# Kernel tuning notes

Hardware: AMD Instinct MI355X
Metric: run time of the kernel (lower is better)

## Reference

```python
import jax, jax.numpy as jnp
import numpy as np

B, T, C, H = 4, 4096, 1024, 16


def setup_inputs() -> dict:
    key = jax.random.key(0)
    k1, k2, k3 = jax.random.split(key, 3)
    x = jax.random.normal(k1, (B, T, C), dtype=jnp.float32)
    # nn.Linear(d_model, 3*d_model, bias=False): weight shape [3C, C]
    W_qkv = jax.random.normal(k2, (3 * C, C), dtype=jnp.float32) * 0.02
    # output Linear(d_model, d_model): weight [C, C], bias [C]
    W_out = jax.random.normal(k3, (C, C), dtype=jnp.float32) * 0.02
    b_out = jnp.zeros((C,), dtype=jnp.float32)
    return {"x": x, "W_qkv": W_qkv, "W_out": W_out, "b_out": b_out}


def reference(x, W_qkv, W_out, b_out):
    Bs, Ts, Cs = x.shape
    dh = Cs // H
    scale = dh ** (-0.5)
    # qkv projection: [B,T,3C]
    qkv = x @ W_qkv.T
    q, k, v = jnp.split(qkv, 3, axis=-1)

    def to_heads(t):  # [B,T,C] -> [B,H,T,dh]
        return t.reshape(Bs, Ts, H, dh).transpose(0, 2, 1, 3)

    q, k, v = to_heads(q), to_heads(k), to_heads(v)
    # rfft over the sequence dim -> [B,H,F,dh], F = T//2+1 (complex64)
    q_f = jnp.fft.rfft(q, axis=-2)
    k_f = jnp.fft.rfft(k, axis=-2)
    # spectral score: sum over head_dim of conj(q)*k, real part -> [B,H,F]
    attn = jnp.sum(jnp.conj(q_f) * k_f, axis=-1).real * scale
    attn = jax.nn.softmax(attn, axis=-1)  # softmax over frequency bins
    v_f = jnp.fft.rfft(v, axis=-2)
    out = jnp.fft.irfft(attn[..., None] * v_f, n=Ts, axis=-2)  # [B,H,T,dh]
    out = out.transpose(0, 2, 1, 3).reshape(Bs, Ts, Cs)
    # output projection (dropout is identity in eval)
    return out @ W_out.T + b_out
```

## Files before the change

### kernel.cpp

```cpp
#include <hip/hip_runtime.h>
#include <math.h>

#define Bsz   4
#define Tsz   4096
#define Csz   1024
#define Hn    16
#define DHn   64
#define NTOT  (Bsz * Tsz)
#define M3    (3 * Csz)
#define Fn    2049
#define BHn   (Bsz * Hn)
#define HALFN 8192

typedef __bf16 bf16x8 __attribute__((ext_vector_type(8)));
typedef __bf16 bf16x4 __attribute__((ext_vector_type(4)));
typedef float  f32x4  __attribute__((ext_vector_type(4)));

#define VMCNT(n) asm volatile("s_waitcnt vmcnt(" #n ")" ::: "memory")
#define LGKM0    asm volatile("s_waitcnt lgkmcnt(0)" ::: "memory")

__device__ __forceinline__ void gload_lds16(const void* g, void* l) {
  __builtin_amdgcn_global_load_lds(
      (const __attribute__((address_space(1))) void*)g,
      (__attribute__((address_space(3))) void*)l, 16, 0, 0);
}

__global__ __launch_bounds__(256)
void cvt_hilo_kernel(const float4* __restrict__ in, bf16x4* __restrict__ hi,
                     bf16x4* __restrict__ lo, int n4) {
  int i = blockIdx.x * blockDim.x + threadIdx.x;
  if (i >= n4) return;
  float4 v = in[i];
  bf16x4 h, l;
  h[0] = (__bf16)v.x; h[1] = (__bf16)v.y; h[2] = (__bf16)v.z; h[3] = (__bf16)v.w;
  l[0] = (__bf16)(v.x - (float)h[0]);
  l[1] = (__bf16)(v.y - (float)h[1]);
  l[2] = (__bf16)(v.z - (float)h[2]);
  l[3] = (__bf16)(v.w - (float)h[3]);
  hi[i] = h;
  lo[i] = l;
}

__global__ __launch_bounds__(256)
void transpose_cvt_kernel(const float* __restrict__ src,
                          __bf16* __restrict__ hi, __bf16* __restrict__ lo) {
  __shared__ float tile[64][65];
  const int tid = threadIdx.x;
  const int n0 = blockIdx.x * 64;
  const int c0 = blockIdx.y * 64;
  const int col = tid & 63;
  const int row4 = tid >> 6;
#pragma unroll
  for (int i = 0; i < 16; ++i) {
    const int r = i * 4 + row4;
    tile[r][col] = src[(size_t)(c0 + r) * NTOT + n0 + col];
  }
  __syncthreads();
#pragma unroll
  for (int i = 0; i < 16; ++i) {
    const int n = i * 4 + row4;
    const float v = tile[col][n];
    const __bf16 h = (__bf16)v;
    const __bf16 l = (__bf16)(v - (float)h);
    hi[(size_t)(n0 + n) * Csz + c0 + col] = h;
    lo[(size_t)(n0 + n) * Csz + c0 + col] = l;
  }
}

template<int COLMAP>
__global__ __launch_bounds__(512, 2)
void gemm_8s(const __bf16* __restrict__ Ahi, const __bf16* __restrict__ Alo,
             const __bf16* __restrict__ Bhi, const __bf16* __restrict__ Blo,
             float* __restrict__ C, int ldC, int nbase,
             const float* __restrict__ bias) {
  __shared__ __align__(16) char lds[131072];

  const int tid  = threadIdx.x;
  const int wid  = tid >> 6;
  const int lane = tid & 63;
  const int wm = wid >> 2, wn = wid & 3;

  int bx = blockIdx.x, by = blockIdx.y;
  {
    const int gx = gridDim.x, gy = gridDim.y;
    const int nwg = gx * gy;
    if ((nwg & 7) == 0) {
      const int flat  = by * gx + bx;
      const int chunk = nwg >> 3;
      const int nf    = (flat & 7) * chunk + (flat >> 3);
      if (COLMAP) { bx = nf / gy; by = nf % gy; }
      else        { bx = nf % gx; by = nf / gx; }
    }
  }
  const int m0 = by * 256;
  const int n0 = bx * 256;

  const int r16 = lane & 15;
  const int kc  = lane >> 4;

  const int aq = (wid & 3) + ((wid & 4) ? 4 : 0);
  const int bq = ((wid & 3) << 1) + (wid >> 2);
  const __bf16* gAh = Ahi + (size_t)(m0 + (wid & 3) * 16 + ((wid & 4) ? 128 : 0) + r16) * Csz + kc * 8;
  const __bf16* gAl = Alo + (size_t)(m0 + (wid & 3) * 16 + ((wid & 4) ? 128 : 0) + r16) * Csz + kc * 8;
  const __bf16* gBh = Bhi + (size_t)(n0 + (wid & 3) * 64 + (wid >> 2) * 16 + r16) * Csz + kc * 8;
  const __bf16* gBl = Blo + (size_t)(n0 + (wid & 3) * 64 + (wid >> 2) * 16 + r16) * Csz + kc * 8;

  auto stA = [&](int h, int ts, char* slot) {
    const size_t o = (size_t)h * 64 * Csz + ts * 32;
    gload_lds16(gAh + o, slot + aq * 1024);
    gload_lds16(gAl + o, slot + 8192 + aq * 1024);
  };
  auto stB = [&](int h, int ts, char* slot) {
    const size_t o = (size_t)h * 32 * Csz + ts * 32;
    gload_lds16(gBh + o, slot + bq * 1024);
    gload_lds16(gBl + o, slot + 8192 + bq * 1024);
  };

  f32x4 acc[8][4];
#pragma unroll
  for (int i = 0; i < 8; ++i)
#pragma unroll
    for (int j = 0; j < 4; ++j) acc[i][j] = (f32x4)(0.f);

  stA(0, 0, lds);            stB(0, 0, lds + 16384);
  stB(1, 0, lds + 32768);    stA(1, 0, lds + 49152);
  stA(0, 1, lds + 65536);    stB(0, 1, lds + 81920);

#pragma unroll 1
  for (int t = 0; t < 32; ++t) {
    char* cur = lds + ((t & 1) << 16);
    char* nxt = lds + (((t & 1) ^ 1) << 16);
    bf16x8 ah[4], al[4], bh[4], bl[4];

    if (t < 31) { VMCNT(8); } else { VMCNT(4); }
    __builtin_amdgcn_s_barrier();
#pragma unroll
    for (int f = 0; f < 4; ++f) {
      const int off = (wm * 4 + f) * 1024 + lane * 16;
      ah[f] = *(const bf16x8*)(cur + off);
      al[f] = *(const bf16x8*)(cur + 8192 + off);
    }
#pragma unroll
    for (int j = 0; j < 2; ++j) {
      const int off = ((wn << 1) + j) * 1024 + lane * 16;
      bh[j] = *(const bf16x8*)(cur + 16384 + off);
      bl[j] = *(const bf16x8*)(cur + 16384 + 8192 + off);
    }
    if (t < 31) stB(1, t + 1, nxt + 32768);
    LGKM0;
    __builtin_amdgcn_sched_barrier(0);
    __builtin_amdgcn_s_setprio(1);
#pragma unroll
    for (int f = 0; f < 4; ++f)
#pragma unroll
      for (int j = 0; j < 2; ++j) {
        f32x4 a_ = acc[f][j];
        a_ = __builtin_amdgcn_mfma_f32_16x16x32_bf16(ah[f], bh[j], a_, 0, 0, 0);
        a_ = __builtin_amdgcn_mfma_f32_16x16x32_bf16(ah[f], bl[j], a_, 0, 0, 0);
        a_ = __builtin_amdgcn_mfma_f32_16x16x32_bf16(al[f], bh[j], a_, 0, 0, 0);
        acc[f][j] = a_;
      }
    __builtin_amdgcn_s_setprio(0);

    if (t < 31) { VMCNT(8); } else { VMCNT(2); }
    __builtin_amdgcn_s_barrier();
#pragma unroll
    for (int j = 0; j < 2; ++j) {
      const int off = ((wn << 1) + j) * 1024 + lane * 16;
      bh[2 + j] = *(const bf16x8*)(cur + 32768 + off);
      bl[2 + j] = *(const bf16x8*)(cur + 32768 + 8192 + off);
    }
    if (t < 31) stA(1, t + 1, nxt + 49152);
    LGKM0;
    __builtin_amdgcn_sched_barrier(0);
    __builtin_amdgcn_s_setprio(1);
#pragma unroll
    for (int f = 0; f < 4; ++f)
#pragma unroll
      for (int j = 0; j < 2; ++j) {
        f32x4 a_ = acc[f][2 + j];
        a_ = __builtin_amdgcn_mfma_f32_16x16x32_bf16(ah[f], bh[2 + j], a_, 0, 0, 0);
        a_ = __builtin_amdgcn_mfma_f32_16x16x32_bf16(ah[f], bl[2 + j], a_, 0, 0, 0);
        a_ = __builtin_amdgcn_mfma_f32_16x16x32_bf16(al[f], bh[2 + j], a_, 0, 0, 0);
        acc[f][2 + j] = a_;
      }
    __builtin_amdgcn_s_setprio(0);

    if (t < 31) { VMCNT(8); } else { VMCNT(0); }
    __builtin_amdgcn_s_barrier();
#pragma unroll
    for (int f = 0; f < 4; ++f) {
      const int off = (wm * 4 + f) * 1024 + lane * 16;
      ah[f] = *(const bf16x8*)(cur + 49152 + off);
      al[f] = *(const bf16x8*)(cur + 49152 + 8192 + off);
    }
    if (t < 30) stA(0, t + 2, cur);
    LGKM0;
    __builtin_amdgcn_sched_barrier(0);
    __builtin_amdgcn_s_setprio(1);
#pragma unroll
    for (int f = 0; f < 4; ++f)
#pragma unroll
      for (int j = 0; j < 2; ++j) {
        f32x4 a_ = acc[4 + f][j];
        a_ = __builtin_amdgcn_mfma_f32_16x16x32_bf16(ah[f], bh[j], a_, 0, 0, 0);
        a_ = __builtin_amdgcn_mfma_f32_16x16x32_bf16(ah[f], bl[j], a_, 0, 0, 0);
        a_ = __builtin_amdgcn_mfma_f32_16x16x32_bf16(al[f], bh[j], a_, 0, 0, 0);
        acc[4 + f][j] = a_;
      }
    __builtin_amdgcn_s_setprio(0);

    __builtin_amdgcn_s_barrier();
    if (t < 30) stB(0, t + 2, cur + 16384);
    __builtin_amdgcn_s_setprio(1);
#pragma unroll
    for (int f = 0; f < 4; ++f)
#pragma unroll
      for (int j = 0; j < 2; ++j) {
        f32x4 a_ = acc[4 + f][2 + j];
        a_ = __builtin_amdgcn_mfma_f32_16x16x32_bf16(ah[f], bh[2 + j], a_, 0, 0, 0);
        a_ = __builtin_amdgcn_mfma_f32_16x16x32_bf16(ah[f], bl[2 + j], a_, 0, 0, 0);
        a_ = __builtin_amdgcn_mfma_f32_16x16x32_bf16(al[f], bh[2 + j], a_, 0, 0, 0);
        acc[4 + f][2 + j] = a_;
      }
    __builtin_amdgcn_s_setprio(0);
  }

  const int cm = m0 + wm * 128 + (lane >> 4) * 4;
  const int cn = nbase + n0 + wn * 64 + (lane & 15);
  float bb[4];
#pragma unroll
  for (int g = 0; g < 4; ++g) bb[g] = bias ? bias[cn - nbase + g * 16] : 0.f;
#pragma unroll
  for (int fm = 0; fm < 8; ++fm)
#pragma unroll
    for (int r = 0; r < 4; ++r) {
      float* cp = C + (size_t)(cm + fm * 16 + r) * ldC + cn;
#pragma unroll
      for (int g = 0; g < 4; ++g) cp[g * 16] = acc[fm][g][r] + bb[g];
    }
}

template<int COLMAP>
__global__ __launch_bounds__(512, 2)
void gemm_8s4(const __bf16* __restrict__ Ahi, const __bf16* __restrict__ Alo,
              const __bf16* __restrict__ Bhi, const __bf16* __restrict__ Blo,
              float* __restrict__ C, int ldC, int nbase,
              const float* __restrict__ bias) {
  __shared__ __align__(16) char lds[98304];

  const int tid  = threadIdx.x;
  const int wid  = tid >> 6;
  const int lane = tid & 63;
  const int wm = wid >> 2, wn = wid & 3;

  int bx = blockIdx.x, by = blockIdx.y;
  {
    const int gx = gridDim.x, gy = gridDim.y;
    const int nwg = gx * gy;
    if ((nwg & 7) == 0) {
      const int flat  = by * gx + bx;
      const int chunk = nwg >> 3;
      const int nf    = (flat & 7) * chunk + (flat >> 3);
      if (COLMAP) { bx = nf / gy; by = nf % gy; }
      else        { bx = nf % gx; by = nf / gx; }
    }
  }
  const int m0 = by * 128;
  const int n0 = bx * 256;

  const int r16 = lane & 15;
  const int kc  = lane >> 4;

  const int cw = wid & 3;
  const __bf16* gA = ((wid & 4) ? Alo : Ahi) +
      (size_t)(m0 + (cw >> 1) * 64 + (cw & 1) * 16 + r16) * Csz + kc * 8;
  const int adst = ((wid & 4) ? 4096 : 0) + cw * 1024;
  const int bq = ((wid & 3) << 1) + (wid >> 2);
  const __bf16* gBh = Bhi + (size_t)(n0 + (wid & 3) * 64 + (wid >> 2) * 16 + r16) * Csz + kc * 8;
  const __bf16* gBl = Blo + (size_t)(n0 + (wid & 3) * 64 + (wid >> 2) * 16 + r16) * Csz + kc * 8;

  auto stA = [&](int h, int ts, char* slot) {
    gload_lds16(gA + (size_t)h * 32 * Csz + ts * 32, slot + adst);
  };
  auto stB = [&](int h, int ts, char* slot) {
    const size_t o = (size_t)h * 32 * Csz + ts * 32;
    gload_lds16(gBh + o, slot + bq * 1024);
    gload_lds16(gBl + o, slot + 8192 + bq * 1024);
  };

  f32x4 acc[4][4];
#pragma unroll
  for (int i = 0; i < 4; ++i)
#pragma unroll
    for (int j = 0; j < 4; ++j) acc[i][j] = (f32x4)(0.f);

  stA(0, 0, lds);            stB(0, 0, lds + 8192);
  stB(1, 0, lds + 24576);    stA(1, 0, lds + 40960);
  stA(0, 1, lds + 49152);    stB(0, 1, lds + 49152 + 8192);

#pragma unroll 1
  for (int t = 0; t < 32; ++t) {
    char* cur = lds + (t & 1) * 49152;
    char* nxt = lds + ((t & 1) ^ 1) * 49152;
    bf16x8 ah[2], al[2], bh[4], bl[4];

    if (t < 31) { VMCNT(6); } else { VMCNT(3); }
    __builtin_amdgcn_s_barrier();
#pragma unroll
    for (int f = 0; f < 2; ++f) {
      const int off = (wm * 2 + f) * 1024 + lane * 16;
      ah[f] = *(const bf16x8*)(cur + off);
      al[f] = *(const bf16x8*)(cur + 4096 + off);
    }
#pragma unroll
    for (int j = 0; j < 2; ++j) {
      const int off = ((wn << 1) + j) * 1024 + lane * 16;
      bh[j] = *(const bf16x8*)(cur + 8192 + off);
      bl[j] = *(const bf16x8*)(cur + 8192 + 8192 + off);
    }
    if (t < 31) stB(1, t + 1, nxt + 24576);
    LGKM0;
    __builtin_amdgcn_sched_barrier(0);
    __builtin_amdgcn_s_setprio(1);
#pragma unroll
    for (int f = 0; f < 2; ++f)
#pragma unroll
      for (int j = 0; j < 2; ++j) {
        f32x4 a_ = acc[f][j];
        a_ = __builtin_amdgcn_mfma_f32_16x16x32_bf16(ah[f], bh[j], a_, 0, 0, 0);
        a_ = __builtin_amdgcn_mfma_f32_16x16x32_bf16(ah[f], bl[j], a_, 0, 0, 0);
        a_ = __builtin_amdgcn_mfma_f32_16x16x32_bf16(al[f], bh[j], a_, 0, 0, 0);
        acc[f][j] = a_;
      }
    __builtin_amdgcn_s_setprio(0);

    if (t < 31) { VMCNT(6); } else { VMCNT(1); }
    __builtin_amdgcn_s_barrier();
#pragma unroll
    for (int j = 0; j < 2; ++j) {
      const int off = ((wn << 1) + j) * 1024 + lane * 16;
      bh[2 + j] = *(const bf16x8*)(cur + 24576 + off);
      bl[2 + j] = *(const bf16x8*)(cur + 24576 + 8192 + off);
    }
    if (t < 31) stA(1, t + 1, nxt + 40960);
    LGKM0;
    __builtin_amdgcn_sched_barrier(0);
    __builtin_amdgcn_s_setprio(1);
#pragma unroll
    for (int f = 0; f < 2; ++f)
#pragma unroll
      for (int j = 0; j < 2; ++j) {
        f32x4 a_ = acc[f][2 + j];
        a_ = __builtin_amdgcn_mfma_f32_16x16x32_bf16(ah[f], bh[2 + j], a_, 0, 0, 0);
        a_ = __builtin_amdgcn_mfma_f32_16x16x32_bf16(ah[f], bl[2 + j], a_, 0, 0, 0);
        a_ = __builtin_amdgcn_mfma_f32_16x16x32_bf16(al[f], bh[2 + j], a_, 0, 0, 0);
        acc[f][2 + j] = a_;
      }
    __builtin_amdgcn_s_setprio(0);

    if (t < 31) { VMCNT(6); } else { VMCNT(0); }
    __builtin_amdgcn_s_barrier();
#pragma unroll
    for (int f = 0; f < 2; ++f) {
      const int off = (wm * 2 + f) * 1024 + lane * 16;
      ah[f] = *(const bf16x8*)(cur + 40960 + off);
      al[f] = *(const bf16x8*)(cur + 40960 + 4096 + off);
    }
    if (t < 30) stA(0, t + 2, cur);
    LGKM0;
    __builtin_amdgcn_sched_barrier(0);
    __builtin_amdgcn_s_setprio(1);
#pragma unroll
    for (int f = 0; f < 2; ++f)
#pragma unroll
      for (int j = 0; j < 2; ++j) {
        f32x4 a_ = acc[2 + f][j];
        a_ = __builtin_amdgcn_mfma_f32_16x16x32_bf16(ah[f], bh[j], a_, 0, 0, 0);
        a_ = __builtin_amdgcn_mfma_f32_16x16x32_bf16(ah[f], bl[j], a_, 0, 0, 0);
        a_ = __builtin_amdgcn_mfma_f32_16x16x32_bf16(al[f], bh[j], a_, 0, 0, 0);
        acc[2 + f][j] = a_;
      }
    __builtin_amdgcn_s_setprio(0);

    __builtin_amdgcn_s_barrier();
    if (t < 30) stB(0, t + 2, cur + 8192);
    __builtin_amdgcn_s_setprio(1);
#pragma unroll
    for (int f = 0; f < 2; ++f)
#pragma unroll
      for (int j = 0; j < 2; ++j) {
        f32x4 a_ = acc[2 + f][2 + j];
        a_ = __builtin_amdgcn_mfma_f32_16x16x32_bf16(ah[f], bh[2 + j], a_, 0, 0, 0);
        a_ = __builtin_amdgcn_mfma_f32_16x16x32_bf16(ah[f], bl[2 + j], a_, 0, 0, 0);
        a_ = __builtin_amdgcn_mfma_f32_16x16x32_bf16(al[f], bh[2 + j], a_, 0, 0, 0);
        acc[2 + f][2 + j] = a_;
      }
    __builtin_amdgcn_s_setprio(0);
  }

  const int cm = m0 + wm * 64 + (lane >> 4) * 4;
  const int cn = nbase + n0 + wn * 64 + (lane & 15);
  float bb[4];
#pragma unroll
  for (int g = 0; g < 4; ++g) bb[g] = bias ? bias[cn - nbase + g * 16] : 0.f;
#pragma unroll
  for (int fm = 0; fm < 4; ++fm)
#pragma unroll
    for (int r = 0; r < 4; ++r) {
      float* cp = C + (size_t)(cm + fm * 16 + r) * ldC + cn;
#pragma unroll
      for (int g = 0; g < 4; ++g) cp[g * 16] = acc[fm][g][r] + bb[g];
    }
}

template<int NT>
__device__ __forceinline__ void build_twiddle(float2* tw, int tid) {
  const float k = 6.28318530717958647692f / 4096.0f;
#pragma unroll
  for (int i = 0; i < 1024 / NT; ++i) {
    const int e = tid + i * NT;
    float sn, cs;
    __sincosf(k * (float)e, &sn, &cs);
    tw[e] = make_float2(cs, sn);
  }
}

__device__ __forceinline__ float2 cmul(float2 a, float2 b) {
  return make_float2(a.x * b.x - a.y * b.y, a.x * b.y + a.y * b.x);
}

template<int NT>
__device__ __forceinline__ void fft4096_r4(float2* X, float2* Y,
                                           const float2* __restrict__ tw,
                                           int tid, float sign) {
  float2* src = X;
  float2* dst = Y;
#pragma unroll 1
  for (int stage = 0; stage < 6; ++stage) {
    const int s = 1 << (2 * stage);
    __syncthreads();
#pragma unroll
    for (int it = 0; it < 1024 / NT; ++it) {
      const int idx = tid + it * NT;
      const int sp = idx & ~(s - 1);
      float2 a0 = src[idx];
      float2 a1 = src[idx + 1024];
      float2 a2 = src[idx + 2048];
      float2 a3 = src[idx + 3072];
      float2 b0 = make_float2(a0.x + a2.x, a0.y + a2.y);
      float2 b1 = make_float2(a0.x - a2.x, a0.y - a2.y);
      float2 b2 = make_float2(a1.x + a3.x, a1.y + a3.y);
      float2 b3 = make_float2(a1.x - a3.x, a1.y - a3.y);
      float2 y0 = make_float2(b0.x + b2.x, b0.y + b2.y);
      float2 y2 = make_float2(b0.x - b2.x, b0.y - b2.y);
      float2 y1 = make_float2(b1.x - sign * b3.y, b1.y + sign * b3.x);
      float2 y3 = make_float2(b1.x + sign * b3.y, b1.y - sign * b3.x);
      float2 w1 = tw[sp];
      w1.y *= sign;
      float2 w2 = make_float2(w1.x * w1.x - w1.y * w1.y, 2.f * w1.x * w1.y);
      float2 w3 = cmul(w1, w2);
      const int o = idx + 3 * sp;
      dst[o]         = y0;
      dst[o + s]     = cmul(w1, y1);
      dst[o + 2 * s] = cmul(w2, y2);
      dst[o + 3 * s] = cmul(w3, y3);
    }
    float2* t = src; src = dst; dst = t;
  }
  __syncthreads();
}

__global__ __launch_bounds__(512)
void qk_cross_kernel(const float* __restrict__ qkT, float* __restrict__ attn_raw,
                     int bhbase) {
  __shared__ float2 bufA[4096];
  __shared__ float2 bufB[4096];
  __shared__ float2 twid[1024];
  const int tid = threadIdx.x;
  const int blk = blockIdx.x;
  const int d = blk & 63;
  const int bh = bhbase + (blk >> 6);
  const int h = bh & 15;
  const int b = bh >> 4;

  build_twiddle<512>(twid, tid);

  const float4* qrow = (const float4*)(qkT + (size_t)(h * DHn + d) * NTOT + b * Tsz);
  const float4* krow = (const float4*)(qkT + (size_t)(Csz + h * DHn + d) * NTOT + b * Tsz);
#pragma unroll
  for (int i = 0; i < 2; ++i) {
    const int t4 = tid + (i << 9);
    float4 qv = qrow[t4];
    float4 kv = krow[t4];
    bufA[t4 * 4 + 0] = make_float2(qv.x, kv.x);
    bufA[t4 * 4 + 1] = make_float2(qv.y, kv.y);
    bufA[t4 * 4 + 2] = make_float2(qv.z, kv.z);
    bufA[t4 * 4 + 3] = make_float2(qv.w, kv.w);
  }

  fft4096_r4<512>(bufA, bufB, twid, tid, -1.0f);

  float* outp = attn_raw + (size_t)bh * Fn;
  for (int f = tid; f < Fn; f += 512) {
    float2 zf = bufA[f];
    float2 zn = bufA[(4096 - f) & 4095];
    float ar = zf.x + zn.x;
    float ai = zf.y - zn.y;
    float br = zf.x - zn.x;
    float bi = zf.y + zn.y;
    float val = 0.03125f * (ar * bi - ai * br);
    atomicAdd(&outp[f], val);
  }
}

__global__ __launch_bounds__(256)
void softmax_kernel(const float* __restrict__ raw, float* __restrict__ attn) {
  __shared__ float red[256];
  const int tid = threadIdx.x;
  const float* in = raw + (size_t)blockIdx.x * Fn;
  float* outp = attn + (size_t)blockIdx.x * Fn;

  float lmax = -3.4e38f;
  for (int f = tid; f < Fn; f += 256) lmax = fmaxf(lmax, in[f]);
  red[tid] = lmax;
  __syncthreads();
  for (int off = 128; off > 0; off >>= 1) {
    if (tid < off) red[tid] = fmaxf(red[tid], red[tid + off]);
    __syncthreads();
  }
  const float mx = red[0];
  __syncthreads();

  float lsum = 0.f;
  for (int f = tid; f < Fn; f += 256) lsum += __expf(in[f] - mx);
  red[tid] = lsum;
  __syncthreads();
  for (int off = 128; off > 0; off >>= 1) {
    if (tid < off) red[tid] += red[tid + off];
    __syncthreads();
  }
  const float inv = 1.0f / red[0];
  for (int f = tid; f < Fn; f += 256) outp[f] = __expf(in[f] - mx) * inv;
}

__global__ __launch_bounds__(512)
void v_filter_kernel(const float* __restrict__ vT, float* __restrict__ vbarT,
                     const float* __restrict__ attn) {
  __shared__ float2 bufA[4096];
  __shared__ float2 bufB[4096];
  __shared__ float2 twid[1024];
  const int tid = threadIdx.x;
  const int blk = blockIdx.x;
  const int jp = blk & 31;
  const int bh = blk >> 5;
  const int h = bh & 15;
  const int b = bh >> 4;
  const int d0 = jp * 2;

  build_twiddle<512>(twid, tid);

  const float4* v0 = (const float4*)(vT + (size_t)(h * DHn + d0) * NTOT + b * Tsz);
  const float4* v1 = (const float4*)(vT + (size_t)(h * DHn + d0 + 1) * NTOT + b * Tsz);
#pragma unroll
  for (int i = 0; i < 2; ++i) {
    const int t4 = tid + (i << 9);
    float4 av = v0[t4];
    float4 bv = v1[t4];
    bufA[t4 * 4 + 0] = make_float2(av.x, bv.x);
    bufA[t4 * 4 + 1] = make_float2(av.y, bv.y);
    bufA[t4 * 4 + 2] = make_float2(av.z, bv.z);
    bufA[t4 * 4 + 3] = make_float2(av.w, bv.w);
  }

  fft4096_r4<512>(bufA, bufB, twid, tid, -1.0f);

  const float* a = attn + (size_t)bh * Fn;
  for (int f = tid; f < 4096; f += 512) {
    int fm = (f <= 2048) ? f : (4096 - f);
    float s = a[fm];
    float2 z = bufA[f];
    bufA[f] = make_float2(z.x * s, z.y * s);
  }

  fft4096_r4<512>(bufA, bufB, twid, tid, +1.0f);

  float* y0 = vbarT + (size_t)(h * DHn + d0) * NTOT + b * Tsz;
  float* y1 = y0 + NTOT;
  const float inv = 1.0f / 4096.0f;
  for (int t = tid; t < 4096; t += 512) {
    float2 z = bufA[t];
    y0[t] = z.x * inv;
    y1[t] = z.y * inv;
  }
}

__global__ void zero_kernel(float* __restrict__ p, int n) {
  int i = blockIdx.x * blockDim.x + threadIdx.x;
  if (i < n) p[i] = 0.f;
}

extern "C" void kernel_launch(void* const* d_in, const int* in_sizes, int n_in,
                              void* d_out, int out_size, void* d_ws, size_t ws_size,
                              hipStream_t stream) {
  const float* x    = (const float*)d_in[0];
  const float* Wqkv = (const float*)d_in[1];
  const float* Wout = (const float*)d_in[2];
  const float* bout = (const float*)d_in[3];
  float* out = (float*)d_out;

  char* ws = (char*)d_ws;
  float* qkT      = (float*)ws;
  float* vT       = (float*)ws;
  __bf16* VThi    = (__bf16*)ws;
  __bf16* VTlo    = (__bf16*)(ws + 33554432ull);
  float* vbarT    = (float*)(ws + 67108864ull);
  float* attn_raw = (float*)(ws + 134217728ull);
  float* attn     = (float*)(ws + 134742272ull);
  __bf16* Whi     = (__bf16*)(ws + 135266816ull);
  __bf16* Wlo     = (__bf16*)(ws + 141558272ull);
  __bf16* Xhi     = (__bf16*)(ws + 147849728ull);
  __bf16* Xlo     = (__bf16*)(ws + 164626944ull);
  __bf16* Wouthi  = (__bf16*)(ws + 181404160ull);
  __bf16* Woutlo  = (__bf16*)(ws + 183501312ull);

  const int nraw = BHn * Fn;
  zero_kernel<<<(nraw + 255) / 256, 256, 0, stream>>>(attn_raw, nraw);

  cvt_hilo_kernel<<<3072, 256, 0, stream>>>((const float4*)Wqkv,
                                            (bf16x4*)Whi, (bf16x4*)Wlo, 786432);
  cvt_hilo_kernel<<<1024, 256, 0, stream>>>((const float4*)Wout,
                                            (bf16x4*)Wouthi, (bf16x4*)Woutlo, 262144);

  for (int half = 0; half < 2; ++half) {
    cvt_hilo_kernel<<<8192, 256, 0, stream>>>(
        (const float4*)(x + (size_t)half * HALFN * Csz),
        (bf16x4*)Xhi, (bf16x4*)Xlo, 2097152);
    gemm_8s<1><<<dim3(32, 8), 512, 0, stream>>>(Whi, Wlo, Xhi, Xlo,
                                                qkT, NTOT, half * HALFN, nullptr);
    qk_cross_kernel<<<2048, 512, 0, stream>>>(qkT, attn_raw, half * 32);
    gemm_8s4<1><<<dim3(32, 8), 512, 0, stream>>>(Whi + 2048 * Csz, Wlo + 2048 * Csz,
                                                 Xhi, Xlo, vT, NTOT, half * HALFN,
                                                 nullptr);
  }

  softmax_kernel<<<BHn, 256, 0, stream>>>(attn_raw, attn);

  v_filter_kernel<<<2048, 512, 0, stream>>>(vT, vbarT, attn);

  transpose_cvt_kernel<<<dim3(NTOT / 64, Csz / 64), 256, 0, stream>>>(vbarT, VThi, VTlo);

  gemm_8s<0><<<dim3(4, 64), 512, 0, stream>>>(VThi, VTlo, Wouthi, Woutlo,
                                              out, Csz, 0, bout);
}
```

Baseline: 553.7 us.

## Switch split-bf16 GEMM to 32x32x16 MFMA tiles with matching LDS layout

Rewrites the main three-pass bf16 hi/lo GEMM to use 32x32x16 MFMA instructions instead of 16x16x32. The global-to-LDS staging layout and the per-wave fragment loads change to feed 32-row tiles, and the epilogue is adapted to the 32x32 accumulator layout. The aim is fewer MFMA issues and fewer LDS fragment reads per FLOP, giving more operand reuse. The cost is a different store pattern in the epilogue and a risk of layout mismatches in the new index math.

```diff
diff --git a/kernel.cpp b/kernel.cpp
--- a/kernel.cpp
+++ b/kernel.cpp
@@ -15,6 +15,7 @@
 typedef __bf16 bf16x8 __attribute__((ext_vector_type(8)));
 typedef __bf16 bf16x4 __attribute__((ext_vector_type(4)));
 typedef float  f32x4  __attribute__((ext_vector_type(4)));
+typedef float  f32x16 __attribute__((ext_vector_type(16)));
 
 #define VMCNT(n) asm volatile("s_waitcnt vmcnt(" #n ")" ::: "memory")
 #define LGKM0    asm volatile("s_waitcnt lgkmcnt(0)" ::: "memory")
@@ -69,7 +70,7 @@
 
 template<int COLMAP>
 __global__ __launch_bounds__(512, 2)
-void gemm_8s(const __bf16* __restrict__ Ahi, const __bf16* __restrict__ Alo,
+void gemm_8w(const __bf16* __restrict__ Ahi, const __bf16* __restrict__ Alo,
              const __bf16* __restrict__ Bhi, const __bf16* __restrict__ Blo,
              float* __restrict__ C, int ldC, int nbase,
              const float* __restrict__ bias) {
@@ -95,20 +96,21 @@
   const int m0 = by * 256;
   const int n0 = bx * 256;
 
-  const int r16 = lane & 15;
-  const int kc  = lane >> 4;
-
-  const int aq = (wid & 3) + ((wid & 4) ? 4 : 0);
-  const int bq = ((wid & 3) << 1) + (wid >> 2);
-  const __bf16* gAh = Ahi + (size_t)(m0 + (wid & 3) * 16 + ((wid & 4) ? 128 : 0) + r16) * Csz + kc * 8;
-  const __bf16* gAl = Alo + (size_t)(m0 + (wid & 3) * 16 + ((wid & 4) ? 128 : 0) + r16) * Csz + kc * 8;
-  const __bf16* gBh = Bhi + (size_t)(n0 + (wid & 3) * 64 + (wid >> 2) * 16 + r16) * Csz + kc * 8;
-  const __bf16* gBl = Blo + (size_t)(n0 + (wid & 3) * 64 + (wid >> 2) * 16 + r16) * Csz + kc * 8;
+  const int r32 = lane & 31;
+  const int kc2 = lane >> 5;
+
+  const __bf16* gAh = Ahi + (size_t)(m0 + (wid >> 2) * 128 + ((wid >> 1) & 1) * 32 + r32) * Csz
+                          + (wid & 1) * 16 + kc2 * 8;
+  const __bf16* gAl = Alo + (size_t)(m0 + (wid >> 2) * 128 + ((wid >> 1) & 1) * 32 + r32) * Csz
+                          + (wid & 1) * 16 + kc2 * 8;
+  const int bq = ((wid & 3) << 1) | (wid >> 2);
+  const __bf16* gBh = Bhi + (size_t)(n0 + (wid & 3) * 64 + r32) * Csz + (wid >> 2) * 16 + kc2 * 8;
+  const __bf16* gBl = Blo + (size_t)(n0 + (wid & 3) * 64 + r32) * Csz + (wid >> 2) * 16 + kc2 * 8;
 
   auto stA = [&](int h, int ts, char* slot) {
     const size_t o = (size_t)h * 64 * Csz + ts * 32;
-    gload_lds16(gAh + o, slot + aq * 1024);
-    gload_lds16(gAl + o, slot + 8192 + aq * 1024);
+    gload_lds16(gAh + o, slot + wid * 1024);
+    gload_lds16(gAl + o, slot + 8192 + wid * 1024);
   };
   auto stB = [&](int h, int ts, char* slot) {
     const size_t o = (size_t)h * 32 * Csz + ts * 32;
@@ -116,128 +118,139 @@
     gload_lds16(gBl + o, slot + 8192 + bq * 1024);
   };
 
-  f32x4 acc[8][4];
-#pragma unroll
-  for (int i = 0; i < 8; ++i)
-#pragma unroll
-    for (int j = 0; j < 4; ++j) acc[i][j] = (f32x4)(0.f);
+  f32x16 acc[4][2];
+#pragma unroll
+  for (int i = 0; i < 4; ++i)
+#pragma unroll
+    for (int j = 0; j < 2; ++j) acc[i][j] = (f32x16)(0.f);
 
   stA(0, 0, lds);            stB(0, 0, lds + 16384);
   stB(1, 0, lds + 32768);    stA(1, 0, lds + 49152);
   stA(0, 1, lds + 65536);    stB(0, 1, lds + 81920);
+
+  bf16x8 ah[2][2], al[2][2], b0h[2], b0l[2], b1h[2], b1l[2];
 
 #pragma unroll 1
   for (int t = 0; t < 32; ++t) {
     char* cur = lds + ((t & 1) << 16);
     char* nxt = lds + (((t & 1) ^ 1) << 16);
-    bf16x8 ah[4], al[4], bh[4], bl[4];
 
     if (t < 31) { VMCNT(8); } else { VMCNT(4); }
     __builtin_amdgcn_s_barrier();
 #pragma unroll
-    for (int f = 0; f < 4; ++f) {
-      const int off = (wm * 4 + f) * 1024 + lane * 16;
-      ah[f] = *(const bf16x8*)(cur + off);
-      al[f] = *(const bf16x8*)(cur + 8192 + off);
-    }
-#pragma unroll
-    for (int j = 0; j < 2; ++j) {
-      const int off = ((wn << 1) + j) * 1024 + lane * 16;
-      bh[j] = *(const bf16x8*)(cur + 16384 + off);
-      bl[j] = *(const bf16x8*)(cur + 16384 + 8192 + off);
+    for (int rt = 0; rt < 2; ++rt)
+#pragma unroll
+      for (int ks = 0; ks < 2; ++ks) {
+        const int off = ((wm << 2) + (rt << 1) + ks) * 1024 + lane * 16;
+        ah[rt][ks] = *(const bf16x8*)(cur + off);
+        al[rt][ks] = *(const bf16x8*)(cur + 8192 + off);
+      }
+#pragma unroll
+    for (int ks = 0; ks < 2; ++ks) {
+      const int off = ((wn << 1) + ks) * 1024 + lane * 16;
+      b0h[ks] = *(const bf16x8*)(cur + 16384 + off);
+      b0l[ks] = *(const bf16x8*)(cur + 16384 + 8192 + off);
     }
     if (t < 31) stB(1, t + 1, nxt + 32768);
     LGKM0;
     __builtin_amdgcn_sched_barrier(0);
     __builtin_amdgcn_s_setprio(1);
 #pragma unroll
-    for (int f = 0; f < 4; ++f)
-#pragma unroll
-      for (int j = 0; j < 2; ++j) {
-        f32x4 a_ = acc[f][j];
-        a_ = __builtin_amdgcn_mfma_f32_16x16x32_bf16(ah[f], bh[j], a_, 0, 0, 0);
-        a_ = __builtin_amdgcn_mfma_f32_16x16x32_bf16(ah[f], bl[j], a_, 0, 0, 0);
-        a_ = __builtin_amdgcn_mfma_f32_16x16x32_bf16(al[f], bh[j], a_, 0, 0, 0);
-        acc[f][j] = a_;
-      }
+    for (int rt = 0; rt < 2; ++rt) {
+      f32x16 a_ = acc[rt][0];
+#pragma unroll
+      for (int ks = 0; ks < 2; ++ks) {
+        a_ = __builtin_amdgcn_mfma_f32_32x32x16_bf16(ah[rt][ks], b0h[ks], a_, 0, 0, 0);
+        a_ = __builtin_amdgcn_mfma_f32_32x32x16_bf16(ah[rt][ks], b0l[ks], a_, 0, 0, 0);
+        a_ = __builtin_amdgcn_mfma_f32_32x32x16_bf16(al[rt][ks], b0h[ks], a_, 0, 0, 0);
+      }
+      acc[rt][0] = a_;
+    }
     __builtin_amdgcn_s_setprio(0);
 
     if (t < 31) { VMCNT(8); } else { VMCNT(2); }
     __builtin_amdgcn_s_barrier();
 #pragma unroll
-    for (int j = 0; j < 2; ++j) {
-      const int off = ((wn << 1) + j) * 1024 + lane * 16;
-      bh[2 + j] = *(const bf16x8*)(cur + 32768 + off);
-      bl[2 + j] = *(const bf16x8*)(cur + 32768 + 8192 + off);
+    for (int ks = 0; ks < 2; ++ks) {
+      const int off = ((wn << 1) + ks) * 1024 + lane * 16;
+      b1h[ks] = *(const bf16x8*)(cur + 32768 + off);
+      b1l[ks] = *(const bf16x8*)(cur + 32768 + 8192 + off);
     }
     if (t < 31) stA(1, t + 1, nxt + 49152);
     LGKM0;
     __builtin_amdgcn_sched_barrier(0);
     __builtin_amdgcn_s_setprio(1);
 #pragma unroll
-    for (int f = 0; f < 4; ++f)
-#pragma unroll
-      for (int j = 0; j < 2; ++j) {
-        f32x4 a_ = acc[f][2 + j];
-        a_ = __builtin_amdgcn_mfma_f32_16x16x32_bf16(ah[f], bh[2 + j], a_, 0, 0, 0);
-        a_ = __builtin_amdgcn_mfma_f32_16x16x32_bf16(ah[f], bl[2 + j], a_, 0, 0, 0);
-        a_ = __builtin_amdgcn_mfma_f32_16x16x32_bf16(al[f], bh[2 + j], a_, 0, 0, 0);
-        acc[f][2 + j] = a_;
-      }
+    for (int rt = 0; rt < 2; ++rt) {
+      f32x16 a_ = acc[rt][1];
+#pragma unroll
+      for (int ks = 0; ks < 2; ++ks) {
+        a_ = __builtin_amdgcn_mfma_f32_32x32x16_bf16(ah[rt][ks], b1h[ks], a_, 0, 0, 0);
+        a_ = __builtin_amdgcn_mfma_f32_32x32x16_bf16(ah[rt][ks], b1l[ks], a_, 0, 0, 0);
+        a_ = __builtin_amdgcn_mfma_f32_32x32x16_bf16(al[rt][ks], b1h[ks], a_, 0, 0, 0);
+      }
+      acc[rt][1] = a_;
+    }
     __builtin_amdgcn_s_setprio(0);
 
     if (t < 31) { VMCNT(8); } else { VMCNT(0); }
     __builtin_amdgcn_s_barrier();
 #pragma unroll
-    for (int f = 0; f < 4; ++f) {
-      const int off = (wm * 4 + f) * 1024 + lane * 16;
-      ah[f] = *(const bf16x8*)(cur + 49152 + off);
-      al[f] = *(const bf16x8*)(cur + 49152 + 8192 + off);
-    }
+    for (int rt = 0; rt < 2; ++rt)
+#pragma unroll
+      for (int ks = 0; ks < 2; ++ks) {
+        const int off = ((wm << 2) + (rt << 1) + ks) * 1024 + lane * 16;
+        ah[rt][ks] = *(const bf16x8*)(cur + 49152 + off);
+        al[rt][ks] = *(const bf16x8*)(cur + 49152 + 8192 + off);
+      }
     if (t < 30) stA(0, t + 2, cur);
     LGKM0;
     __builtin_amdgcn_sched_barrier(0);
     __builtin_amdgcn_s_setprio(1);
 #pragma unroll
-    for (int f = 0; f < 4; ++f)
-#pragma unroll
-      for (int j = 0; j < 2; ++j) {
-        f32x4 a_ = acc[4 + f][j];
-        a_ = __builtin_amdgcn_mfma_f32_16x16x32_bf16(ah[f], bh[j], a_, 0, 0, 0);
-        a_ = __builtin_amdgcn_mfma_f32_16x16x32_bf16(ah[f], bl[j], a_, 0, 0, 0);
-        a_ = __builtin_amdgcn_mfma_f32_16x16x32_bf16(al[f], bh[j], a_, 0, 0, 0);
-        acc[4 + f][j] = a_;
-      }
+    for (int rt = 0; rt < 2; ++rt) {
+      f32x16 a_ = acc[2 + rt][0];
+#pragma unroll
+      for (int ks = 0; ks < 2; ++ks) {
+        a_ = __builtin_amdgcn_mfma_f32_32x32x16_bf16(ah[rt][ks], b0h[ks], a_, 0, 0, 0);
+        a_ = __builtin_amdgcn_mfma_f32_32x32x16_bf16(ah[rt][ks], b0l[ks], a_, 0, 0, 0);
+        a_ = __builtin_amdgcn_mfma_f32_32x32x16_bf16(al[rt][ks], b0h[ks], a_, 0, 0, 0);
+      }
+      acc[2 + rt][0] = a_;
+    }
     __builtin_amdgcn_s_setprio(0);
 
     __builtin_amdgcn_s_barrier();
     if (t < 30) stB(0, t + 2, cur + 16384);
     __builtin_amdgcn_s_setprio(1);
 #pragma unroll
-    for (int f = 0; f < 4; ++f)
-#pragma unroll
-      for (int j = 0; j < 2; ++j) {
-        f32x4 a_ = acc[4 + f][2 + j];
-        a_ = __builtin_amdgcn_mfma_f32_16x16x32_bf16(ah[f], bh[2 + j], a_, 0, 0, 0);
-        a_ = __builtin_amdgcn_mfma_f32_16x16x32_bf16(ah[f], bl[2 + j], a_, 0, 0, 0);
-        a_ = __builtin_amdgcn_mfma_f32_16x16x32_bf16(al[f], bh[2 + j], a_, 0, 0, 0);
-        acc[4 + f][2 + j] = a_;
-      }
-    __builtin_amdgcn_s_setprio(0);
-  }
-
-  const int cm = m0 + wm * 128 + (lane >> 4) * 4;
-  const int cn = nbase + n0 + wn * 64 + (lane & 15);
-  float bb[4];
-#pragma unroll
-  for (int g = 0; g < 4; ++g) bb[g] = bias ? bias[cn - nbase + g * 16] : 0.f;
-#pragma unroll
-  for (int fm = 0; fm < 8; ++fm)
-#pragma unroll
-    for (int r = 0; r < 4; ++r) {
-      float* cp = C + (size_t)(cm + fm * 16 + r) * ldC + cn;
-#pragma unroll
-      for (int g = 0; g < 4; ++g) cp[g * 16] = acc[fm][g][r] + bb[g];
+    for (int rt = 0; rt < 2; ++rt) {
+      f32x16 a_ = acc[2 + rt][1];
+#pragma unroll
+      for (int ks = 0; ks < 2; ++ks) {
+        a_ = __builtin_amdgcn_mfma_f32_32x32x16_bf16(ah[rt][ks], b1h[ks], a_, 0, 0, 0);
+        a_ = __builtin_amdgcn_mfma_f32_32x32x16_bf16(ah[rt][ks], b1l[ks], a_, 0, 0, 0);
+        a_ = __builtin_amdgcn_mfma_f32_32x32x16_bf16(al[rt][ks], b1h[ks], a_, 0, 0, 0);
+      }
+      acc[2 + rt][1] = a_;
+    }
+    __builtin_amdgcn_s_setprio(0);
+  }
+
+  const int coll  = lane & 31;
+  const int rbase = (lane >> 5) * 4;
+  const int cnb   = nbase + n0 + wn * 64;
+#pragma unroll
+  for (int RT = 0; RT < 4; ++RT)
+#pragma unroll
+    for (int ct = 0; ct < 2; ++ct) {
+      const float bb = bias ? bias[n0 + wn * 64 + ct * 32 + coll] : 0.f;
+      const int mb = m0 + wm * 128 + RT * 32 + rbase;
+#pragma unroll
+      for (int r = 0; r < 16; ++r) {
+        const int row = (r & 3) + ((r >> 2) << 3);
+        C[(size_t)(mb + row) * ldC + cnb + ct * 32 + coll] = acc[RT][ct][r] + bb;
+      }
     }
 }
 
@@ -636,7 +649,7 @@
     cvt_hilo_kernel<<<8192, 256, 0, stream>>>(
         (const float4*)(x + (size_t)half * HALFN * Csz),
         (bf16x4*)Xhi, (bf16x4*)Xlo, 2097152);
-    gemm_8s<1><<<dim3(32, 8), 512, 0, stream>>>(Whi, Wlo, Xhi, Xlo,
+    gemm_8w<1><<<dim3(32, 8), 512, 0, stream>>>(Whi, Wlo, Xhi, Xlo,
                                                 qkT, NTOT, half * HALFN, nullptr);
     qk_cross_kernel<<<2048, 512, 0, stream>>>(qkT, attn_raw, half * 32);
     gemm_8s4<1><<<dim3(32, 8), 512, 0, stream>>>(Whi + 2048 * Csz, Wlo + 2048 * Csz,
@@ -650,6 +663,6 @@
 
   transpose_cvt_kernel<<<dim3(NTOT / 64, Csz / 64), 256, 0, stream>>>(vbarT, VThi, VTlo);
 
-  gemm_8s<0><<<dim3(4, 64), 512, 0, stream>>>(VThi, VTlo, Wouthi, Woutlo,
+  gemm_8w<0><<<dim3(4, 64), 512, 0, stream>>>(VThi, VTlo, Wouthi, Woutlo,
                                               out, Csz, 0, bout);
 }
```

New measurement: 590.7 us. 1.07x slower.
